# Kernel optimization log

Hardware: AMD Instinct MI355X
Metric: run time of the kernel (lower is better)

Reference implementation:

```python
import jax, jax.numpy as jnp
import numpy as np

D_MODEL = 256
POOL = 10  # Keras MaxPooling1D(pool_size=10) -> stride 10, padding 'same'


def setup_inputs() -> dict:
    key = jax.random.key(0)
    ks = jax.random.split(key, 11)
    B, S, D = 4, 4096, D_MODEL
    scale = 1.0 / np.sqrt(D)
    inp = {
        "v": jax.random.normal(ks[0], (B, S, D), jnp.float32),
        "k": jax.random.normal(ks[1], (B, S, D), jnp.float32),
        "q": jax.random.normal(ks[2], (B, S, D), jnp.float32),
        "wq": jax.random.normal(ks[3], (D, D), jnp.float32) * scale,
        "bq": jnp.zeros((D,), jnp.float32),
        "wk": jax.random.normal(ks[4], (D, D), jnp.float32) * scale,
        "bk": jnp.zeros((D,), jnp.float32),
        "wv": jax.random.normal(ks[5], (D, D), jnp.float32) * scale,
        "bv": jnp.zeros((D,), jnp.float32),
        "wo": jax.random.normal(ks[6], (D, D), jnp.float32) * scale,
        "bo": jnp.zeros((D,), jnp.float32),
    }
    return inp


def reference(v, k, q, wq, bq, wk, bk, wv, bv, wo, bo):
    d = q.shape[-1]
    qp = q @ wq + bq          # [B,Sq,D]
    kp = k @ wk + bk          # [B,Sk,D]
    vp = v @ wv + bv          # [B,Sk,D]
    scores = jnp.einsum('bqd,bkd->bqk', qp, kp) / jnp.sqrt(jnp.float32(d))
    # MaxPooling1D over the steps (Sq) axis, stride = pool_size, 'same' padding
    pooled = jax.lax.reduce_window(
        scores, -jnp.inf, jax.lax.max,
        window_dimensions=(1, POOL, 1),
        window_strides=(1, POOL, 1),
        padding='SAME')          # [B, ceil(Sq/10), Sk]
    attn = jax.nn.softmax(pooled, axis=-1)
    out = jnp.einsum('bqk,bkd->bqd', attn, vp)
    return out @ wo + bo
```

## Files before the change

### kernel.cpp

```cpp
#include <hip/hip_runtime.h>
#include <hip/hip_bf16.h>
#include <stdint.h>

typedef __attribute__((ext_vector_type(8))) short          bf16x8;
typedef __attribute__((ext_vector_type(4))) float          f32x4;
typedef __attribute__((ext_vector_type(4))) float          f4;
typedef __attribute__((ext_vector_type(8))) unsigned short u16x8;
typedef __attribute__((ext_vector_type(4))) unsigned short u16x4;

#define DEVINL __device__ __forceinline__

static constexpr int B  = 4;
static constexpr int S  = 4096;
static constexpr int D  = 256;
static constexpr int SP = 410;
static constexpr int KZ = 16;
static constexpr int MO = B * SP;
static constexpr size_t PSLICE = (size_t)MO * D;

DEVINL unsigned short f2bf(float x) {
  union { float f; unsigned u; } v; v.f = x;
  unsigned r = v.u + 0x7FFFu + ((v.u >> 16) & 1u);
  return (unsigned short)(r >> 16);
}

DEVINL f32x4 mfma16(bf16x8 a, bf16x8 b, f32x4 c) {
  return __builtin_amdgcn_mfma_f32_16x16x32_bf16(a, b, c, 0, 0, 0);
}

typedef const __attribute__((address_space(1))) void* gas_t;
typedef __attribute__((address_space(3))) void*       las_t;
DEVINL void gload16(const void* g, void* l) {
  __builtin_amdgcn_global_load_lds((gas_t)g, (las_t)l, 16, 0, 0);
}

DEVINL void cfence() { asm volatile("" ::: "memory"); }
DEVINL void barrier_mem() { cfence(); __builtin_amdgcn_s_barrier(); cfence(); }
#define WAIT_VM(N) asm volatile("s_waitcnt vmcnt(" #N ")" ::: "memory")

__global__ __launch_bounds__(256) void wt_trans_kernel(
    const float* __restrict__ wq, const float* __restrict__ wk,
    const float* __restrict__ wv, const float* __restrict__ wo,
    unsigned short* __restrict__ wt)
{
  int idx = blockIdx.x * 256 + threadIdx.x;
  int mat = idx >> 16;
  int r   = idx & 65535;
  int n   = r >> 8;
  int k   = r & 255;
  const float* w = (mat == 0) ? wq : (mat == 1) ? wk : (mat == 2) ? wv : wo;
  wt[idx] = f2bf(w[k * 256 + n]);
}

__global__ __launch_bounds__(256) void cvt_kernel(
    const float* __restrict__ xq, const float* __restrict__ xk, const float* __restrict__ xv,
    unsigned short* __restrict__ oq, unsigned short* __restrict__ ok, unsigned short* __restrict__ ov)
{
  int z = blockIdx.y;
  const float* x    = (z == 0) ? xq : (z == 1) ? xk : xv;
  unsigned short* o = (z == 0) ? oq : (z == 1) ? ok : ov;
  size_t i = ((size_t)blockIdx.x * 256 + threadIdx.x) * 8;
  f4 a = *reinterpret_cast<const f4*>(x + i);
  f4 c = *reinterpret_cast<const f4*>(x + i + 4);
  u16x8 h;
  h[0] = f2bf(a[0]); h[1] = f2bf(a[1]); h[2] = f2bf(a[2]); h[3] = f2bf(a[3]);
  h[4] = f2bf(c[0]); h[5] = f2bf(c[1]); h[6] = f2bf(c[2]); h[7] = f2bf(c[3]);
  *reinterpret_cast<u16x8*>(o + i) = h;
}

__global__ __launch_bounds__(512) void proj_kernel(
    const unsigned short* __restrict__ xq, const unsigned short* __restrict__ xk,
    const unsigned short* __restrict__ xv, const unsigned short* __restrict__ wt,
    const float* __restrict__ bq, const float* __restrict__ bk, const float* __restrict__ bv,
    unsigned short* __restrict__ qp, unsigned short* __restrict__ kp, unsigned short* __restrict__ vp)
{
  int z = blockIdx.z;
  const unsigned short* X = (z == 0) ? xq : (z == 1) ? xk : xv;
  const unsigned short* W = wt + z * 65536;
  const float* bias       = (z == 0) ? bq : (z == 1) ? bk : bv;
  unsigned short* Out     = (z == 0) ? qp : (z == 1) ? kp : vp;

  int m0 = blockIdx.x * 256;
  int n0 = blockIdx.y * 128;

  __shared__ __align__(16) struct { char A[2][32768]; char Bm[2][16384]; } sm;

  const char* Xc = (const char*)X;
  const char* Wc = (const char*)W;

  int tid  = threadIdx.x;
  int lane = tid & 63, wid = tid >> 6;
  int wr = wid >> 1, wc = wid & 1;
  int lrow = lane & 15, kseg = lane >> 4;

  f32x4 zero4 = {0.f, 0.f, 0.f, 0.f};
  f32x4 acc[4][4];
#pragma unroll
  for (int i = 0; i < 4; i++)
#pragma unroll
    for (int j = 0; j < 4; j++) acc[i][j] = zero4;

  auto stage = [&](int t, int buf) {
#pragma unroll
    for (int i = 0; i < 4; ++i) {
      int inst = wid * 4 + i;
      int sg   = inst * 64 + lane;
      int row  = sg >> 3, c16 = sg & 7;
      gload16(Xc + ((size_t)(m0 + row) << 9) + (t << 7) + ((c16 ^ (row & 7)) << 4),
              sm.A[buf] + inst * 1024);
    }
#pragma unroll
    for (int i = 0; i < 2; ++i) {
      int inst = wid * 2 + i;
      int sg   = inst * 64 + lane;
      int row  = sg >> 3, c16 = sg & 7;
      gload16(Wc + ((size_t)(n0 + row) << 9) + (t << 7) + ((c16 ^ (row & 7)) << 4),
              sm.Bm[buf] + inst * 1024);
    }
  };

  stage(0, 0);
#pragma unroll
  for (int t = 0; t < 4; ++t) {
    int cur = t & 1;
    if (t < 3) { stage(t + 1, cur ^ 1); WAIT_VM(6); } else { WAIT_VM(0); }
    barrier_mem();
    const char* Asm = sm.A[cur];
    const char* Bsm = sm.Bm[cur];
#pragma unroll
    for (int kk = 0; kk < 2; ++kk) {
      bf16x8 af[4], bfr[4];
#pragma unroll
      for (int mi = 0; mi < 4; ++mi) {
        int R = wr * 64 + mi * 16 + lrow;
        int c16 = (kk * 4 + kseg) ^ (R & 7);
        af[mi] = *reinterpret_cast<const bf16x8*>(Asm + R * 128 + c16 * 16);
      }
#pragma unroll
      for (int cf = 0; cf < 4; ++cf) {
        int nl = wc * 64 + cf * 16 + lrow;
        int c16 = (kk * 4 + kseg) ^ (nl & 7);
        bfr[cf] = *reinterpret_cast<const bf16x8*>(Bsm + nl * 128 + c16 * 16);
      }
#pragma unroll
      for (int mi = 0; mi < 4; ++mi)
#pragma unroll
        for (int cf = 0; cf < 4; ++cf)
          acc[mi][cf] = mfma16(af[mi], bfr[cf], acc[mi][cf]);
    }
    barrier_mem();
  }

  int r4 = kseg * 4;
#pragma unroll
  for (int mi = 0; mi < 4; mi++)
#pragma unroll
    for (int cf = 0; cf < 4; cf++) {
      int n = n0 + wc * 64 + cf * 16 + lrow;
      float bv_ = bias[n];
#pragma unroll
      for (int r = 0; r < 4; r++) {
        int m = m0 + wr * 64 + mi * 16 + r4 + r;
        Out[(size_t)m * 256 + n] = f2bf(acc[mi][cf][r] + bv_);
      }
    }
}

__global__ __launch_bounds__(512) void scores_pool_kernel(
    const unsigned short* __restrict__ qp, const unsigned short* __restrict__ kp,
    float* __restrict__ pooled)
{
  int b  = blockIdx.z;
  int wb = blockIdx.y;
  int nb = blockIdx.x;
  int w0 = wb * 25;
  int qb = w0 * 10 - 2;
  int n0 = nb * 128;
  int nwin = SP - w0; if (nwin > 25) nwin = 25;

  __shared__ __align__(16) union SM {
    struct { char A[2][32768]; char Bm[2][16384]; } st;
    float pm[9216];
  } sm;

  const char* qpc = (const char*)(qp + (size_t)b * S * 256);
  const char* kpc = (const char*)(kp + (size_t)b * S * 256);

  int tid  = threadIdx.x;
  int lane = tid & 63, wid = tid >> 6;
  int wr = wid >> 1, wc = wid & 1;
  int lrow = lane & 15, kseg = lane >> 4;

  f32x4 zero4 = {0.f, 0.f, 0.f, 0.f};
  f32x4 acc[4][4];
#pragma unroll
  for (int i = 0; i < 4; i++)
#pragma unroll
    for (int j = 0; j < 4; j++) acc[i][j] = zero4;

  auto stage = [&](int t, int buf) {
#pragma unroll
    for (int i = 0; i < 4; ++i) {
      int inst = wid * 4 + i;
      int sg   = inst * 64 + lane;
      int row  = sg >> 3, c16 = sg & 7;
      int q = qb + row; q = (q < 0) ? 0 : ((q > S - 1) ? (S - 1) : q);
      gload16(qpc + ((size_t)q << 9) + (t << 7) + ((c16 ^ (row & 7)) << 4),
              sm.st.A[buf] + inst * 1024);
    }
#pragma unroll
    for (int i = 0; i < 2; ++i) {
      int inst = wid * 2 + i;
      int sg   = inst * 64 + lane;
      int row  = sg >> 3, c16 = sg & 7;
      gload16(kpc + ((size_t)(n0 + row) << 9) + (t << 7) + ((c16 ^ (row & 7)) << 4),
              sm.st.Bm[buf] + inst * 1024);
    }
  };

  stage(0, 0);
#pragma unroll
  for (int t = 0; t < 4; ++t) {
    int cur = t & 1;
    if (t < 3) { stage(t + 1, cur ^ 1); WAIT_VM(6); } else { WAIT_VM(0); }
    barrier_mem();
    const char* Asm = sm.st.A[cur];
    const char* Bsm = sm.st.Bm[cur];
#pragma unroll
    for (int kk = 0; kk < 2; ++kk) {
      bf16x8 af[4], bfr[4];
#pragma unroll
      for (int mi = 0; mi < 4; ++mi) {
        int R = wr * 64 + mi * 16 + lrow;
        int c16 = (kk * 4 + kseg) ^ (R & 7);
        af[mi] = *reinterpret_cast<const bf16x8*>(Asm + R * 128 + c16 * 16);
      }
#pragma unroll
      for (int cf = 0; cf < 4; ++cf) {
        int nl = wc * 64 + cf * 16 + lrow;
        int c16 = (kk * 4 + kseg) ^ (nl & 7);
        bfr[cf] = *reinterpret_cast<const bf16x8*>(Bsm + nl * 128 + c16 * 16);
      }
#pragma unroll
      for (int mi = 0; mi < 4; ++mi)
#pragma unroll
        for (int cf = 0; cf < 4; ++cf)
          acc[mi][cf] = mfma16(af[mi], bfr[cf], acc[mi][cf]);
    }
    barrier_mem();
  }

  int h = kseg;
#pragma unroll
  for (int c = 0; c < 2; ++c) {
    __syncthreads();
    if (wc == c) {
#pragma unroll
      for (int mi = 0; mi < 4; ++mi) {
        int p = wr * 32 + mi * 8 + h * 2;
#pragma unroll
        for (int cf = 0; cf < 4; ++cf) {
          int col = cf * 16 + lrow;
          sm.pm[p * 72 + col]       = fmaxf(acc[mi][cf][0], acc[mi][cf][1]);
          sm.pm[(p + 1) * 72 + col] = fmaxf(acc[mi][cf][2], acc[mi][cf][3]);
        }
      }
    }
    __syncthreads();
    for (int s = tid; s < 1600; s += 512) {
      int j = s >> 6, col = s & 63;
      if (j < nwin) {
        float m = -3.4e38f;
#pragma unroll
        for (int i = 0; i < 5; ++i) {
          int p  = 5 * j + i;
          int q0 = qb + 2 * p;
          if (q0 >= 0 && q0 < S) m = fmaxf(m, sm.pm[p * 72 + col]);
        }
        pooled[((size_t)b * SP + w0 + j) * 4096 + n0 + c * 64 + col] = m * 0.0625f;
      }
    }
  }
}

__global__ __launch_bounds__(256) void softmax_kernel(
    const float* __restrict__ pooled, unsigned short* __restrict__ attn)
{
  int row = blockIdx.x;
  const float* p = pooled + (size_t)row * 4096;
  unsigned short* a = attn + (size_t)row * 4096;
  int tid = threadIdx.x;
  int lane = tid & 63, wid = tid >> 6;

  f4 v[4];
  float mx = -3.4e38f;
#pragma unroll
  for (int i = 0; i < 4; i++) {
    v[i] = *reinterpret_cast<const f4*>(&p[i * 1024 + tid * 4]);
    mx = fmaxf(mx, fmaxf(fmaxf(v[i][0], v[i][1]), fmaxf(v[i][2], v[i][3])));
  }
#pragma unroll
  for (int off = 32; off > 0; off >>= 1) mx = fmaxf(mx, __shfl_xor(mx, off, 64));
  __shared__ float redm[4];
  __shared__ float reds[4];
  if (lane == 0) redm[wid] = mx;
  __syncthreads();
  mx = fmaxf(fmaxf(redm[0], redm[1]), fmaxf(redm[2], redm[3]));

  float e[16];
  float sum = 0.f;
#pragma unroll
  for (int i = 0; i < 4; i++)
#pragma unroll
    for (int j = 0; j < 4; j++) {
      float t = __expf(v[i][j] - mx);
      e[i * 4 + j] = t;
      sum += t;
    }
#pragma unroll
  for (int off = 32; off > 0; off >>= 1) sum += __shfl_xor(sum, off, 64);
  if (lane == 0) reds[wid] = sum;
  __syncthreads();
  sum = reds[0] + reds[1] + reds[2] + reds[3];
  float inv = 1.f / sum;
#pragma unroll
  for (int i = 0; i < 4; i++) {
    u16x4 o;
#pragma unroll
    for (int j = 0; j < 4; j++) o[j] = f2bf(e[i * 4 + j] * inv);
    *reinterpret_cast<u16x4*>(&a[i * 1024 + tid * 4]) = o;
  }
}

__global__ __launch_bounds__(256) void vpt_kernel(
    const unsigned short* __restrict__ vp, unsigned short* __restrict__ vpT)
{
  int b  = blockIdx.y;
  int kt = blockIdx.x >> 2;
  int dt = blockIdx.x & 3;
  int k0 = kt * 64, d0 = dt * 64;

  __shared__ unsigned short t[64][66];
  const unsigned short* src = vp + (size_t)b * S * 256;
  unsigned short* dst = vpT + (size_t)b * 256 * S;

  int tid = threadIdx.x;
  for (int s = tid; s < 512; s += 256) {
    int r = s >> 3, seg = s & 7;
    u16x8 v = *reinterpret_cast<const u16x8*>(&src[(size_t)(k0 + r) * 256 + d0 + seg * 8]);
#pragma unroll
    for (int j = 0; j < 4; j++) {
      unsigned short* pp = &t[r][seg * 8 + j * 2];
      pp[0] = v[j * 2]; pp[1] = v[j * 2 + 1];
    }
  }
  __syncthreads();
  int d  = tid >> 2;
  int kb = (tid & 3) * 16;
  u16x8 o0, o1;
#pragma unroll
  for (int j = 0; j < 8; j++) o0[j] = t[kb + j][d];
#pragma unroll
  for (int j = 0; j < 8; j++) o1[j] = t[kb + 8 + j][d];
  *reinterpret_cast<u16x8*>(&dst[(size_t)(d0 + d) * S + k0 + kb])     = o0;
  *reinterpret_cast<u16x8*>(&dst[(size_t)(d0 + d) * S + k0 + kb + 8]) = o1;
}

__global__ __launch_bounds__(256) void pv_kernel(
    const unsigned short* __restrict__ attn, const unsigned short* __restrict__ vpT,
    float* __restrict__ part)
{
  int bx = blockIdx.x;
  int b  = bx >> 2, mt = bx & 3;
  int m0 = mt * 128;
  int n0 = blockIdx.y * 128;
  int kz = blockIdx.z;
  int k0b = kz * 512;

  const char* Ac = (const char*)(attn + (size_t)b * SP * 4096);
  const char* Bc = (const char*)(vpT  + (size_t)b * 256 * 4096);
  float* Pz = part + (size_t)kz * PSLICE;

  __shared__ __align__(16) struct { char A[2][16384]; char Bm[2][16384]; } sm;

  int tid  = threadIdx.x;
  int lane = tid & 63, wid = tid >> 6;
  int wr = wid >> 1, wc = wid & 1;
  int lrow = lane & 15, kseg = lane >> 4;

  f32x4 zero4 = {0.f, 0.f, 0.f, 0.f};
  f32x4 acc[4][4];
#pragma unroll
  for (int i = 0; i < 4; i++)
#pragma unroll
    for (int j = 0; j < 4; j++) acc[i][j] = zero4;

  auto stage = [&](int t, int buf) {
#pragma unroll
    for (int i = 0; i < 4; ++i) {
      int inst = wid * 4 + i;
      int sg   = inst * 64 + lane;
      int row  = sg >> 3, c16 = sg & 7;
      int m = m0 + row; m = (m > SP - 1) ? (SP - 1) : m;
      gload16(Ac + (size_t)m * 8192 + k0b + (t << 7) + ((c16 ^ (row & 7)) << 4),
              sm.A[buf] + inst * 1024);
    }
#pragma unroll
    for (int i = 0; i < 4; ++i) {
      int inst = wid * 4 + i;
      int sg   = inst * 64 + lane;
      int row  = sg >> 3, c16 = sg & 7;
      gload16(Bc + (size_t)(n0 + row) * 8192 + k0b + (t << 7) + ((c16 ^ (row & 7)) << 4),
              sm.Bm[buf] + inst * 1024);
    }
  };

  stage(0, 0);
#pragma unroll
  for (int t = 0; t < 4; ++t) {
    int cur = t & 1;
    if (t < 3) { stage(t + 1, cur ^ 1); WAIT_VM(8); } else { WAIT_VM(0); }
    barrier_mem();
    const char* Asm = sm.A[cur];
    const char* Bsm = sm.Bm[cur];
#pragma unroll
    for (int kk = 0; kk < 2; ++kk) {
      bf16x8 af[4], bfr[4];
#pragma unroll
      for (int mi = 0; mi < 4; ++mi) {
        int R = wr * 64 + mi * 16 + lrow;
        int c16 = (kk * 4 + kseg) ^ (R & 7);
        af[mi] = *reinterpret_cast<const bf16x8*>(Asm + R * 128 + c16 * 16);
      }
#pragma unroll
      for (int cf = 0; cf < 4; ++cf) {
        int nl = wc * 64 + cf * 16 + lrow;
        int c16 = (kk * 4 + kseg) ^ (nl & 7);
        bfr[cf] = *reinterpret_cast<const bf16x8*>(Bsm + nl * 128 + c16 * 16);
      }
#pragma unroll
      for (int mi = 0; mi < 4; ++mi)
#pragma unroll
        for (int cf = 0; cf < 4; ++cf)
          acc[mi][cf] = mfma16(af[mi], bfr[cf], acc[mi][cf]);
    }
    barrier_mem();
  }

  int r4 = kseg * 4;
#pragma unroll
  for (int mi = 0; mi < 4; mi++)
#pragma unroll
    for (int cf = 0; cf < 4; cf++) {
      int n = n0 + wc * 64 + cf * 16 + lrow;
#pragma unroll
      for (int r = 0; r < 4; r++) {
        int m = m0 + wr * 64 + mi * 16 + r4 + r;
        if (m < SP) Pz[((size_t)b * SP + m) * 256 + n] = acc[mi][cf][r];
      }
    }
}

__global__ __launch_bounds__(256) void reduce_kernel(
    const float* __restrict__ part, unsigned short* __restrict__ ctxb)
{
  size_t i = (size_t)blockIdx.x * 256 + threadIdx.x;
  float s = 0.f;
#pragma unroll
  for (int z = 0; z < KZ; ++z) s += part[z * PSLICE + i];
  ctxb[i] = f2bf(s);
}

__global__ __launch_bounds__(512) void out_kernel(
    const unsigned short* __restrict__ ctxb, const unsigned short* __restrict__ woT,
    const float* __restrict__ bo, float* __restrict__ out)
{
  int m0 = blockIdx.x * 256;
  int n0 = blockIdx.y * 128;

  __shared__ __align__(16) struct { char A[2][32768]; char Bm[2][16384]; } sm;

  const char* Xc = (const char*)ctxb;
  const char* Wc = (const char*)woT;

  int tid  = threadIdx.x;
  int lane = tid & 63, wid = tid >> 6;
  int wr = wid >> 1, wc = wid & 1;
  int lrow = lane & 15, kseg = lane >> 4;

  f32x4 zero4 = {0.f, 0.f, 0.f, 0.f};
  f32x4 acc[4][4];
#pragma unroll
  for (int i = 0; i < 4; i++)
#pragma unroll
    for (int j = 0; j < 4; j++) acc[i][j] = zero4;

  auto stage = [&](int t, int buf) {
#pragma unroll
    for (int i = 0; i < 4; ++i) {
      int inst = wid * 4 + i;
      int sg   = inst * 64 + lane;
      int row  = sg >> 3, c16 = sg & 7;
      int m = m0 + row; m = (m > MO - 1) ? (MO - 1) : m;
      gload16(Xc + ((size_t)m << 9) + (t << 7) + ((c16 ^ (row & 7)) << 4),
              sm.A[buf] + inst * 1024);
    }
#pragma unroll
    for (int i = 0; i < 2; ++i) {
      int inst = wid * 2 + i;
      int sg   = inst * 64 + lane;
      int row  = sg >> 3, c16 = sg & 7;
      gload16(Wc + ((size_t)(n0 + row) << 9) + (t << 7) + ((c16 ^ (row & 7)) << 4),
              sm.Bm[buf] + inst * 1024);
    }
  };

  stage(0, 0);
#pragma unroll
  for (int t = 0; t < 4; ++t) {
    int cur = t & 1;
    if (t < 3) { stage(t + 1, cur ^ 1); WAIT_VM(6); } else { WAIT_VM(0); }
    barrier_mem();
    const char* Asm = sm.A[cur];
    const char* Bsm = sm.Bm[cur];
#pragma unroll
    for (int kk = 0; kk < 2; ++kk) {
      bf16x8 af[4], bfr[4];
#pragma unroll
      for (int mi = 0; mi < 4; ++mi) {
        int R = wr * 64 + mi * 16 + lrow;
        int c16 = (kk * 4 + kseg) ^ (R & 7);
        af[mi] = *reinterpret_cast<const bf16x8*>(Asm + R * 128 + c16 * 16);
      }
#pragma unroll
      for (int cf = 0; cf < 4; ++cf) {
        int nl = wc * 64 + cf * 16 + lrow;
        int c16 = (kk * 4 + kseg) ^ (nl & 7);
        bfr[cf] = *reinterpret_cast<const bf16x8*>(Bsm + nl * 128 + c16 * 16);
      }
#pragma unroll
      for (int mi = 0; mi < 4; ++mi)
#pragma unroll
        for (int cf = 0; cf < 4; ++cf)
          acc[mi][cf] = mfma16(af[mi], bfr[cf], acc[mi][cf]);
    }
    barrier_mem();
  }

  int r4 = kseg * 4;
#pragma unroll
  for (int mi = 0; mi < 4; mi++)
#pragma unroll
    for (int cf = 0; cf < 4; cf++) {
      int n = n0 + wc * 64 + cf * 16 + lrow;
      float bv_ = bo[n];
#pragma unroll
      for (int r = 0; r < 4; r++) {
        int m = m0 + wr * 64 + mi * 16 + r4 + r;
        if (m < MO) out[(size_t)m * 256 + n] = acc[mi][cf][r] + bv_;
      }
    }
}

extern "C" void kernel_launch(void* const* d_in, const int* in_sizes, int n_in,
                              void* d_out, int out_size, void* d_ws, size_t ws_size,
                              hipStream_t stream)
{
  const float* v  = (const float*)d_in[0];
  const float* k  = (const float*)d_in[1];
  const float* q  = (const float*)d_in[2];
  const float* wq = (const float*)d_in[3];
  const float* bq = (const float*)d_in[4];
  const float* wk = (const float*)d_in[5];
  const float* bk = (const float*)d_in[6];
  const float* wv = (const float*)d_in[7];
  const float* bv = (const float*)d_in[8];
  const float* wo = (const float*)d_in[9];
  const float* bo = (const float*)d_in[10];
  float* out = (float*)d_out;

  char* ws = (char*)d_ws;
  size_t off = 0;
  auto alloc = [&](size_t bytes) -> void* {
    void* p = ws + off;
    off += (bytes + 255) & ~(size_t)255;
    return p;
  };
  unsigned short* qp   = (unsigned short*)alloc((size_t)B * S * D * 2);
  unsigned short* kp   = (unsigned short*)alloc((size_t)B * S * D * 2);
  unsigned short* vp   = (unsigned short*)alloc((size_t)B * S * D * 2);
  unsigned short* vpT  = (unsigned short*)alloc((size_t)B * S * D * 2);
  unsigned short* wt   = (unsigned short*)alloc((size_t)4 * 256 * 256 * 2);
  unsigned short* ctxb = (unsigned short*)alloc(PSLICE * 2);
  char* shared_region  = (char*)alloc((size_t)B * SP * 4096 * 4);
  unsigned short* attn = (unsigned short*)alloc((size_t)B * SP * 4096 * 2);

  unsigned short* qx = (unsigned short*)shared_region;
  unsigned short* kx = qx + (size_t)B * S * D;
  unsigned short* vx = kx + (size_t)B * S * D;
  float* pooled = (float*)shared_region;
  float* part   = (float*)shared_region;

  wt_trans_kernel<<<1024, 256, 0, stream>>>(wq, wk, wv, wo, wt);
  cvt_kernel<<<dim3(2048, 3), 256, 0, stream>>>(q, k, v, qx, kx, vx);
  proj_kernel<<<dim3(64, 2, 3), 512, 0, stream>>>(qx, kx, vx, wt, bq, bk, bv, qp, kp, vp);
  scores_pool_kernel<<<dim3(32, 17, 4), 512, 0, stream>>>(qp, kp, pooled);
  softmax_kernel<<<B * SP, 256, 0, stream>>>(pooled, attn);
  vpt_kernel<<<dim3(256, 4), 256, 0, stream>>>(vp, vpT);
  pv_kernel<<<dim3(16, 2, KZ), 256, 0, stream>>>(attn, vpT, part);
  reduce_kernel<<<(int)(PSLICE / 256), 256, 0, stream>>>(part, ctxb);
  out_kernel<<<dim3(7, 2), 512, 0, stream>>>(ctxb, wt + 3 * 65536, bo, out);
}
```

Measured before the change: 231.2 us.

## Fuse weight and input conversion, write V transposed from projection, persist scores blocks

Merges the weight-transpose and activation-conversion launches into one kernel. The V projection epilogue now writes its output already transposed, which removes the separate transpose kernel and its intermediate buffer. The scores/pool kernel becomes persistent over window blocks: each block loads its full 128x256 K tile into LDS once and loops over 8-9 query windows, staging only Q. This cuts K reloads and launch count, but the V stores become strided 8-byte writes and the grid shrinks to 256 blocks, which may lower occupancy.

After: 221.9 us. 1.04x faster.

```diff
diff --git a/kernel.cpp b/kernel.cpp
--- a/kernel.cpp
+++ b/kernel.cpp
@@ -36,27 +36,32 @@
 
 DEVINL void cfence() { asm volatile("" ::: "memory"); }
 DEVINL void barrier_mem() { cfence(); __builtin_amdgcn_s_barrier(); cfence(); }
+DEVINL void lds_barrier() {
+  asm volatile("s_waitcnt lgkmcnt(0)" ::: "memory");
+  __builtin_amdgcn_s_barrier();
+  cfence();
+}
 #define WAIT_VM(N) asm volatile("s_waitcnt vmcnt(" #N ")" ::: "memory")
 
-__global__ __launch_bounds__(256) void wt_trans_kernel(
+__global__ __launch_bounds__(256) void cvtwt_kernel(
+    const float* __restrict__ xq, const float* __restrict__ xk, const float* __restrict__ xv,
     const float* __restrict__ wq, const float* __restrict__ wk,
     const float* __restrict__ wv, const float* __restrict__ wo,
+    unsigned short* __restrict__ oq, unsigned short* __restrict__ ok, unsigned short* __restrict__ ov,
     unsigned short* __restrict__ wt)
 {
-  int idx = blockIdx.x * 256 + threadIdx.x;
-  int mat = idx >> 16;
-  int r   = idx & 65535;
-  int n   = r >> 8;
-  int k   = r & 255;
-  const float* w = (mat == 0) ? wq : (mat == 1) ? wk : (mat == 2) ? wv : wo;
-  wt[idx] = f2bf(w[k * 256 + n]);
-}
-
-__global__ __launch_bounds__(256) void cvt_kernel(
-    const float* __restrict__ xq, const float* __restrict__ xk, const float* __restrict__ xv,
-    unsigned short* __restrict__ oq, unsigned short* __restrict__ ok, unsigned short* __restrict__ ov)
-{
   int z = blockIdx.y;
+  if (z == 3) {
+    if (blockIdx.x >= 1024) return;
+    int idx = blockIdx.x * 256 + threadIdx.x;
+    int mat = idx >> 16;
+    int r   = idx & 65535;
+    int n   = r >> 8;
+    int k   = r & 255;
+    const float* w = (mat == 0) ? wq : (mat == 1) ? wk : (mat == 2) ? wv : wo;
+    wt[idx] = f2bf(w[k * 256 + n]);
+    return;
+  }
   const float* x    = (z == 0) ? xq : (z == 1) ? xk : xv;
   unsigned short* o = (z == 0) ? oq : (z == 1) ? ok : ov;
   size_t i = ((size_t)blockIdx.x * 256 + threadIdx.x) * 8;
@@ -72,13 +77,12 @@
     const unsigned short* __restrict__ xq, const unsigned short* __restrict__ xk,
     const unsigned short* __restrict__ xv, const unsigned short* __restrict__ wt,
     const float* __restrict__ bq, const float* __restrict__ bk, const float* __restrict__ bv,
-    unsigned short* __restrict__ qp, unsigned short* __restrict__ kp, unsigned short* __restrict__ vp)
+    unsigned short* __restrict__ qp, unsigned short* __restrict__ kp, unsigned short* __restrict__ vpT)
 {
   int z = blockIdx.z;
   const unsigned short* X = (z == 0) ? xq : (z == 1) ? xk : xv;
   const unsigned short* W = wt + z * 65536;
   const float* bias       = (z == 0) ? bq : (z == 1) ? bk : bv;
-  unsigned short* Out     = (z == 0) ? qp : (z == 1) ? kp : vp;
 
   int m0 = blockIdx.x * 256;
   int n0 = blockIdx.y * 128;
@@ -152,36 +156,51 @@
   }
 
   int r4 = kseg * 4;
-#pragma unroll
-  for (int mi = 0; mi < 4; mi++)
-#pragma unroll
-    for (int cf = 0; cf < 4; cf++) {
-      int n = n0 + wc * 64 + cf * 16 + lrow;
-      float bv_ = bias[n];
-#pragma unroll
-      for (int r = 0; r < 4; r++) {
-        int m = m0 + wr * 64 + mi * 16 + r4 + r;
-        Out[(size_t)m * 256 + n] = f2bf(acc[mi][cf][r] + bv_);
-      }
-    }
+  if (z < 2) {
+    unsigned short* Out = (z == 0) ? qp : kp;
+#pragma unroll
+    for (int mi = 0; mi < 4; mi++)
+#pragma unroll
+      for (int cf = 0; cf < 4; cf++) {
+        int n = n0 + wc * 64 + cf * 16 + lrow;
+        float bv_ = bias[n];
+#pragma unroll
+        for (int r = 0; r < 4; r++) {
+          int m = m0 + wr * 64 + mi * 16 + r4 + r;
+          Out[(size_t)m * 256 + n] = f2bf(acc[mi][cf][r] + bv_);
+        }
+      }
+  } else {
+#pragma unroll
+    for (int mi = 0; mi < 4; mi++)
+#pragma unroll
+      for (int cf = 0; cf < 4; cf++) {
+        int n = n0 + wc * 64 + cf * 16 + lrow;
+        float bv_ = bias[n];
+        u16x4 hh;
+#pragma unroll
+        for (int r = 0; r < 4; r++) hh[r] = f2bf(acc[mi][cf][r] + bv_);
+        int m  = m0 + wr * 64 + mi * 16 + r4;
+        int bb = m >> 12, s = m & 4095;
+        *reinterpret_cast<u16x4*>(&vpT[(size_t)bb * (256 * 4096) + (size_t)n * 4096 + s]) = hh;
+      }
+  }
 }
 
 __global__ __launch_bounds__(512) void scores_pool_kernel(
     const unsigned short* __restrict__ qp, const unsigned short* __restrict__ kp,
     float* __restrict__ pooled)
 {
-  int b  = blockIdx.z;
-  int wb = blockIdx.y;
-  int nb = blockIdx.x;
-  int w0 = wb * 25;
-  int qb = w0 * 10 - 2;
-  int n0 = nb * 128;
-  int nwin = SP - w0; if (nwin > 25) nwin = 25;
-
-  __shared__ __align__(16) union SM {
-    struct { char A[2][32768]; char Bm[2][16384]; } st;
-    float pm[9216];
-  } sm;
+  int id   = blockIdx.x;
+  int nb   = id & 31;
+  int b    = (id >> 5) & 3;
+  int half = id >> 7;
+  int wb0  = half ? 9 : 0;
+  int nwb  = half ? 8 : 9;
+  int n0   = nb * 128;
+
+  __shared__ __align__(16) struct { char A[2][32768]; char Bm[65536]; } sm;
+  float* pm = (float*)sm.A[1];
 
   const char* qpc = (const char*)(qp + (size_t)b * S * 256);
   const char* kpc = (const char*)(kp + (size_t)b * S * 256);
@@ -190,95 +209,110 @@
   int lane = tid & 63, wid = tid >> 6;
   int wr = wid >> 1, wc = wid & 1;
   int lrow = lane & 15, kseg = lane >> 4;
-
-  f32x4 zero4 = {0.f, 0.f, 0.f, 0.f};
-  f32x4 acc[4][4];
-#pragma unroll
-  for (int i = 0; i < 4; i++)
-#pragma unroll
-    for (int j = 0; j < 4; j++) acc[i][j] = zero4;
-
-  auto stage = [&](int t, int buf) {
+  int h = kseg;
+
+#pragma unroll
+  for (int i = 0; i < 8; ++i) {
+    int inst = wid * 8 + i;
+    int sg   = inst * 64 + lane;
+    int row  = sg >> 5, c16 = sg & 31;
+    gload16(kpc + ((size_t)(n0 + row) << 9) + (((size_t)(c16 ^ (row & 7))) << 4),
+            sm.Bm + inst * 1024);
+  }
+
+  auto stageA = [&](int qbt, int ks, int buf) {
 #pragma unroll
     for (int i = 0; i < 4; ++i) {
       int inst = wid * 4 + i;
       int sg   = inst * 64 + lane;
       int row  = sg >> 3, c16 = sg & 7;
-      int q = qb + row; q = (q < 0) ? 0 : ((q > S - 1) ? (S - 1) : q);
-      gload16(qpc + ((size_t)q << 9) + (t << 7) + ((c16 ^ (row & 7)) << 4),
-              sm.st.A[buf] + inst * 1024);
-    }
-#pragma unroll
-    for (int i = 0; i < 2; ++i) {
-      int inst = wid * 2 + i;
-      int sg   = inst * 64 + lane;
-      int row  = sg >> 3, c16 = sg & 7;
-      gload16(kpc + ((size_t)(n0 + row) << 9) + (t << 7) + ((c16 ^ (row & 7)) << 4),
-              sm.st.Bm[buf] + inst * 1024);
+      int q = qbt + row; q = (q < 0) ? 0 : ((q > S - 1) ? (S - 1) : q);
+      gload16(qpc + ((size_t)q << 9) + (ks << 7) + ((c16 ^ (row & 7)) << 4),
+              sm.A[buf] + inst * 1024);
     }
   };
 
-  stage(0, 0);
-#pragma unroll
-  for (int t = 0; t < 4; ++t) {
-    int cur = t & 1;
-    if (t < 3) { stage(t + 1, cur ^ 1); WAIT_VM(6); } else { WAIT_VM(0); }
-    barrier_mem();
-    const char* Asm = sm.st.A[cur];
-    const char* Bsm = sm.st.Bm[cur];
-#pragma unroll
-    for (int kk = 0; kk < 2; ++kk) {
-      bf16x8 af[4], bfr[4];
-#pragma unroll
-      for (int mi = 0; mi < 4; ++mi) {
-        int R = wr * 64 + mi * 16 + lrow;
-        int c16 = (kk * 4 + kseg) ^ (R & 7);
-        af[mi] = *reinterpret_cast<const bf16x8*>(Asm + R * 128 + c16 * 16);
-      }
-#pragma unroll
-      for (int cf = 0; cf < 4; ++cf) {
-        int nl = wc * 64 + cf * 16 + lrow;
-        int c16 = (kk * 4 + kseg) ^ (nl & 7);
-        bfr[cf] = *reinterpret_cast<const bf16x8*>(Bsm + nl * 128 + c16 * 16);
-      }
-#pragma unroll
-      for (int mi = 0; mi < 4; ++mi)
-#pragma unroll
-        for (int cf = 0; cf < 4; ++cf)
-          acc[mi][cf] = mfma16(af[mi], bfr[cf], acc[mi][cf]);
-    }
-    barrier_mem();
-  }
-
-  int h = kseg;
-#pragma unroll
-  for (int c = 0; c < 2; ++c) {
-    __syncthreads();
-    if (wc == c) {
-#pragma unroll
-      for (int mi = 0; mi < 4; ++mi) {
-        int p = wr * 32 + mi * 8 + h * 2;
+  stageA(wb0 * 250 - 2, 0, 0);
+
+  int gmax = nwb * 4;
+  for (int i = 0; i < nwb; ++i) {
+    int wb = wb0 + i, w0 = wb * 25;
+    int qb = w0 * 10 - 2;
+    int nwin = SP - w0; if (nwin > 25) nwin = 25;
+
+    f32x4 zero4 = {0.f, 0.f, 0.f, 0.f};
+    f32x4 acc[4][4];
+#pragma unroll
+    for (int mi = 0; mi < 4; mi++)
+#pragma unroll
+      for (int cf = 0; cf < 4; cf++) acc[mi][cf] = zero4;
+
+#pragma unroll
+    for (int ks = 0; ks < 4; ++ks) {
+      int g  = (i << 2) | ks;
+      int gn = g + 1;
+      if (gn < gmax) {
+        int i2 = gn >> 2, ks2 = gn & 3;
+        stageA((wb0 + i2) * 250 - 2, ks2, gn & 1);
+        WAIT_VM(4);
+      } else {
+        WAIT_VM(0);
+      }
+      barrier_mem();
+      const char* Asm = sm.A[g & 1];
+#pragma unroll
+      for (int kk = 0; kk < 2; ++kk) {
+        bf16x8 af[4], bfr[4];
+#pragma unroll
+        for (int mi = 0; mi < 4; ++mi) {
+          int R = wr * 64 + mi * 16 + lrow;
+          int c16 = (kk * 4 + kseg) ^ (R & 7);
+          af[mi] = *reinterpret_cast<const bf16x8*>(Asm + R * 128 + c16 * 16);
+        }
 #pragma unroll
         for (int cf = 0; cf < 4; ++cf) {
-          int col = cf * 16 + lrow;
-          sm.pm[p * 72 + col]       = fmaxf(acc[mi][cf][0], acc[mi][cf][1]);
-          sm.pm[(p + 1) * 72 + col] = fmaxf(acc[mi][cf][2], acc[mi][cf][3]);
+          int nl = wc * 64 + cf * 16 + lrow;
+          int c16 = ((ks << 3) + kk * 4 + kseg) ^ (nl & 7);
+          bfr[cf] = *reinterpret_cast<const bf16x8*>(sm.Bm + nl * 512 + c16 * 16);
         }
-      }
-    }
-    __syncthreads();
-    for (int s = tid; s < 1600; s += 512) {
-      int j = s >> 6, col = s & 63;
-      if (j < nwin) {
-        float m = -3.4e38f;
-#pragma unroll
-        for (int i = 0; i < 5; ++i) {
-          int p  = 5 * j + i;
-          int q0 = qb + 2 * p;
-          if (q0 >= 0 && q0 < S) m = fmaxf(m, sm.pm[p * 72 + col]);
+#pragma unroll
+        for (int mi = 0; mi < 4; ++mi)
+#pragma unroll
+          for (int cf = 0; cf < 4; ++cf)
+            acc[mi][cf] = mfma16(af[mi], bfr[cf], acc[mi][cf]);
+      }
+      barrier_mem();
+    }
+
+#pragma unroll
+    for (int c = 0; c < 2; ++c) {
+      if (wc == c) {
+#pragma unroll
+        for (int mi = 0; mi < 4; ++mi) {
+          int p = wr * 32 + mi * 8 + h * 2;
+#pragma unroll
+          for (int cf = 0; cf < 4; ++cf) {
+            int col = cf * 16 + lrow;
+            pm[p * 64 + col]       = fmaxf(acc[mi][cf][0], acc[mi][cf][1]);
+            pm[(p + 1) * 64 + col] = fmaxf(acc[mi][cf][2], acc[mi][cf][3]);
+          }
         }
-        pooled[((size_t)b * SP + w0 + j) * 4096 + n0 + c * 64 + col] = m * 0.0625f;
-      }
+      }
+      lds_barrier();
+      for (int s = tid; s < 1600; s += 512) {
+        int j = s >> 6, col = s & 63;
+        if (j < nwin) {
+          float m = -3.4e38f;
+#pragma unroll
+          for (int t5 = 0; t5 < 5; ++t5) {
+            int p  = 5 * j + t5;
+            int q0 = qb + 2 * p;
+            if (q0 >= 0 && q0 < S) m = fmaxf(m, pm[p * 64 + col]);
+          }
+          pooled[((size_t)b * SP + w0 + j) * 4096 + n0 + c * 64 + col] = m * 0.0625f;
+        }
+      }
+      lds_barrier();
     }
   }
 }
@@ -330,40 +364,6 @@
     for (int j = 0; j < 4; j++) o[j] = f2bf(e[i * 4 + j] * inv);
     *reinterpret_cast<u16x4*>(&a[i * 1024 + tid * 4]) = o;
   }
-}
-
-__global__ __launch_bounds__(256) void vpt_kernel(
-    const unsigned short* __restrict__ vp, unsigned short* __restrict__ vpT)
-{
-  int b  = blockIdx.y;
-  int kt = blockIdx.x >> 2;
-  int dt = blockIdx.x & 3;
-  int k0 = kt * 64, d0 = dt * 64;
-
-  __shared__ unsigned short t[64][66];
-  const unsigned short* src = vp + (size_t)b * S * 256;
-  unsigned short* dst = vpT + (size_t)b * 256 * S;
-
-  int tid = threadIdx.x;
-  for (int s = tid; s < 512; s += 256) {
-    int r = s >> 3, seg = s & 7;
-    u16x8 v = *reinterpret_cast<const u16x8*>(&src[(size_t)(k0 + r) * 256 + d0 + seg * 8]);
-#pragma unroll
-    for (int j = 0; j < 4; j++) {
-      unsigned short* pp = &t[r][seg * 8 + j * 2];
-      pp[0] = v[j * 2]; pp[1] = v[j * 2 + 1];
-    }
-  }
-  __syncthreads();
-  int d  = tid >> 2;
-  int kb = (tid & 3) * 16;
-  u16x8 o0, o1;
-#pragma unroll
-  for (int j = 0; j < 8; j++) o0[j] = t[kb + j][d];
-#pragma unroll
-  for (int j = 0; j < 8; j++) o1[j] = t[kb + 8 + j][d];
-  *reinterpret_cast<u16x8*>(&dst[(size_t)(d0 + d) * S + k0 + kb])     = o0;
-  *reinterpret_cast<u16x8*>(&dst[(size_t)(d0 + d) * S + k0 + kb + 8]) = o1;
 }
 
 __global__ __launch_bounds__(256) void pv_kernel(
@@ -588,7 +588,6 @@
   };
   unsigned short* qp   = (unsigned short*)alloc((size_t)B * S * D * 2);
   unsigned short* kp   = (unsigned short*)alloc((size_t)B * S * D * 2);
-  unsigned short* vp   = (unsigned short*)alloc((size_t)B * S * D * 2);
   unsigned short* vpT  = (unsigned short*)alloc((size_t)B * S * D * 2);
   unsigned short* wt   = (unsigned short*)alloc((size_t)4 * 256 * 256 * 2);
   unsigned short* ctxb = (unsigned short*)alloc(PSLICE * 2);
@@ -601,12 +600,10 @@
   float* pooled = (float*)shared_region;
   float* part   = (float*)shared_region;
 
-  wt_trans_kernel<<<1024, 256, 0, stream>>>(wq, wk, wv, wo, wt);
-  cvt_kernel<<<dim3(2048, 3), 256, 0, stream>>>(q, k, v, qx, kx, vx);
-  proj_kernel<<<dim3(64, 2, 3), 512, 0, stream>>>(qx, kx, vx, wt, bq, bk, bv, qp, kp, vp);
-  scores_pool_kernel<<<dim3(32, 17, 4), 512, 0, stream>>>(qp, kp, pooled);
+  cvtwt_kernel<<<dim3(2048, 4), 256, 0, stream>>>(q, k, v, wq, wk, wv, wo, qx, kx, vx, wt);
+  proj_kernel<<<dim3(64, 2, 3), 512, 0, stream>>>(qx, kx, vx, wt, bq, bk, bv, qp, kp, vpT);
+  scores_pool_kernel<<<256, 512, 0, stream>>>(qp, kp, pooled);
   softmax_kernel<<<B * SP, 256, 0, stream>>>(pooled, attn);
-  vpt_kernel<<<dim3(256, 4), 256, 0, stream>>>(vp, vpT);
   pv_kernel<<<dim3(16, 2, KZ), 256, 0, stream>>>(attn, vpT, part);
   reduce_kernel<<<(int)(PSLICE / 256), 256, 0, stream>>>(part, ctxb);
   out_kernel<<<dim3(7, 2), 512, 0, stream>>>(ctxb, wt + 3 * 65536, bo, out);
```
